# Kernel optimization log

Hardware: AMD Instinct MI355X
Metric: run time of the kernel (lower is better)

The kernel has to match this reference:

```python
import jax, jax.numpy as jnp
import numpy as np

N, B, E = 10000, 4, 160000
C_IN, C_OUT, C_E = 64, 64, 16


def _mk_params(key, c_in, c_out, c_e):
    ks = jax.random.split(key, 8)
    s = 0.1
    return dict(
        w_n=jax.random.normal(ks[0], (c_in, c_out), jnp.float32) * s,
        w_e=jax.random.normal(ks[1], (c_e, c_out), jnp.float32) * s,
        q=jax.random.normal(ks[2], (c_out, c_out), jnp.float32) * s,
        k=jax.random.normal(ks[3], (c_out, c_out), jnp.float32) * s,
        aw=jax.random.normal(ks[4], (3 * c_out, 1), jnp.float32) * s,
        ab=jax.random.normal(ks[5], (1,), jnp.float32) * s,
        ow=jax.random.normal(ks[6], (2 * c_out, c_out), jnp.float32) * s,
        ob=jax.random.normal(ks[7], (c_out,), jnp.float32) * s,
    )


def setup_inputs() -> dict:
    key = jax.random.key(0)
    kx, ke, ka, k1, k2 = jax.random.split(key, 5)
    inp = {
        'X': jax.random.normal(kx, (N, B, C_IN), jnp.float32),
        'edge_index': jax.random.randint(ke, (2, E), 0, N, jnp.int32),
        'edge_attr': jax.random.normal(ka, (E, C_E), jnp.float32),
    }
    p1 = _mk_params(k1, C_IN, C_OUT, C_E)
    p2 = _mk_params(k2, C_OUT, C_OUT, C_E)
    for name, v in p1.items():
        inp[name + '1'] = v
    for name, v in p2.items():
        inp[name + '2'] = v
    return inp


def egnn_conv(x, edge_index, edge_attr, w_n, w_e, q, k, aw, ab, ow, ob, n_nodes):
    # x: [N,B,Cin]; edge_attr: [E,Ce]
    xp = x @ w_n                         # [N,B,C]
    ea = edge_attr @ w_e                 # [E,C]
    src, dst = edge_index[0], edge_index[1]
    xj = xp[src]                         # [E,B,C] gather (source)
    xi = xp[dst]                         # [E,B,C] gather (target)
    qf = xj @ q                          # [E,B,C]
    kf = xi @ k                          # [E,B,C]
    eab = jnp.broadcast_to(ea[:, None, :], qf.shape)  # [E,B,C]
    att_feat = jnp.concatenate([qf, kf, eab], axis=-1)  # [E,B,3C]
    att = jax.nn.sigmoid(att_feat @ aw + ab)            # [E,B,1]
    gate = jax.nn.sigmoid(eab)
    msg = att * xj * gate                # [E,B,C]
    aggr = jax.ops.segment_max(msg, dst, num_segments=n_nodes)  # [N,B,C]
    aggr = jnp.where(jnp.isneginf(aggr), 0.0, aggr)  # empty segments -> 0
    out = jnp.concatenate([xp, aggr], axis=-1) @ ow + ob
    return xp + out


def reference(X, edge_index, edge_attr,
              w_n1, w_e1, q1, k1, aw1, ab1, ow1, ob1,
              w_n2, w_e2, q2, k2, aw2, ab2, ow2, ob2):
    n_nodes = X.shape[0]
    c1 = egnn_conv(X, edge_index, edge_attr, w_n1, w_e1, q1, k1, aw1, ab1, ow1, ob1, n_nodes)
    c1 = jax.nn.leaky_relu(c1, 0.01)
    c2 = egnn_conv(c1, edge_index, edge_attr, w_n2, w_e2, q2, k2, aw2, ab2, ow2, ob2, n_nodes)
    c2 = jax.nn.leaky_relu(c2, 0.01)
    return c2
```

## Files before the change

### kernel.cpp

```cpp
#include <hip/hip_runtime.h>
#include <math.h>

#define NN 10000
#define BB 4
#define EE 160000
#define CC 64
#define CE 16

static constexpr size_t OFF_XPA    = 0;
static constexpr size_t OFF_XPB    = 10240000;
static constexpr size_t OFF_SA     = 20480000;
static constexpr size_t OFF_SB     = 20640000;
static constexpr size_t OFF_VECS   = 20800000;
static constexpr size_t OFF_COUNTS = 20801280;
static constexpr size_t OFF_CURSOR = 20841280;
static constexpr size_t OFF_OFFS   = 20881280;
static constexpr size_t OFF_RECS   = 20921344;
static constexpr size_t OFF_ATT    = 22201344;
static constexpr size_t OFF_SE12   = 24761344;
static constexpr size_t OFF_ORDER  = 26041344;

__device__ __forceinline__ float sigmoidf_(float x) {
    return __builtin_amdgcn_rcpf(1.0f + __expf(-x));
}

__device__ __forceinline__ float bcast_(float v, int l) {
    return __uint_as_float(__builtin_amdgcn_readlane(__float_as_uint(v), l));
}

__global__ void hist_vecs_kernel(const int* __restrict__ ei, int* __restrict__ counts,
                                 const float* __restrict__ q1, const float* __restrict__ k1,
                                 const float* __restrict__ aw1, const float* __restrict__ we1,
                                 const float* __restrict__ q2, const float* __restrict__ k2,
                                 const float* __restrict__ aw2, const float* __restrict__ we2,
                                 float* __restrict__ vecs) {
    int e = blockIdx.x * blockDim.x + threadIdx.x;
    if (e < EE) atomicAdd(&counts[ei[EE + e]], 1);
    if (blockIdx.x == 0) {
        int t = threadIdx.x;
        if (t < 64) {
            float a = 0.f, b = 0.f, c = 0.f, d = 0.f;
            for (int j = 0; j < 64; ++j) {
                a = fmaf(q1[t * 64 + j], aw1[j], a);
                b = fmaf(k1[t * 64 + j], aw1[64 + j], b);
                c = fmaf(q2[t * 64 + j], aw2[j], c);
                d = fmaf(k2[t * 64 + j], aw2[64 + j], d);
            }
            vecs[t] = a; vecs[64 + t] = b; vecs[144 + t] = c; vecs[208 + t] = d;
        }
        if (t < 16) {
            float a = 0.f, b = 0.f;
            for (int j = 0; j < 64; ++j) {
                a = fmaf(we1[t * 64 + j], aw1[128 + j], a);
                b = fmaf(we2[t * 64 + j], aw2[128 + j], b);
            }
            vecs[128 + t] = a; vecs[272 + t] = b;
        }
    }
}

__global__ __launch_bounds__(1024) void scan_order_kernel(const int* __restrict__ counts,
                                                          int* __restrict__ offs,
                                                          int* __restrict__ order) {
    __shared__ int hist[1024];
    __shared__ int cur[1024];
    __shared__ int startb[1024];
    __shared__ int wsum[16];
    int t = threadIdx.x;
    hist[t] = 0; cur[t] = 0;
    int lane = t & 63, wid = t >> 6;
    int v[10];
    int s = 0;
    #pragma unroll
    for (int j = 0; j < 10; ++j) {
        int i = t * 10 + j;
        v[j] = (i < NN) ? counts[i] : 0;
        s += v[j];
    }
    int ps = s;
    #pragma unroll
    for (int off = 1; off < 64; off <<= 1) {
        int u = __shfl_up(ps, off, 64);
        if (lane >= off) ps += u;
    }
    if (lane == 63) wsum[wid] = ps;
    __syncthreads();
    int wbase = 0;
    for (int w = 0; w < wid; ++w) wbase += wsum[w];
    int tb = wbase + ps - s;
    #pragma unroll
    for (int j = 0; j < 10; ++j) {
        int i = t * 10 + j;
        if (i < NN) offs[i] = tb;
        tb += v[j];
    }
    if (t == 1023) offs[NN] = tb;
    #pragma unroll
    for (int j = 0; j < 10; ++j) {
        int i = t * 10 + j;
        if (i < NN) {
            int d = v[j] > 1023 ? 1023 : v[j];
            atomicAdd(&hist[d], 1);
        }
    }
    __syncthreads();
    int r = 1023 - t;
    int hv = hist[r];
    int ps2 = hv;
    #pragma unroll
    for (int off = 1; off < 64; off <<= 1) {
        int u = __shfl_up(ps2, off, 64);
        if (lane >= off) ps2 += u;
    }
    if (lane == 63) wsum[wid] = ps2;
    __syncthreads();
    int wb2 = 0;
    for (int w = 0; w < wid; ++w) wb2 += wsum[w];
    startb[r] = wb2 + ps2 - hv;
    __syncthreads();
    #pragma unroll
    for (int j = 0; j < 10; ++j) {
        int i = t * 10 + j;
        if (i < NN) {
            int d = v[j] > 1023 ? 1023 : v[j];
            int pos = startb[d] + atomicAdd(&cur[d], 1);
            order[pos] = i;
        }
    }
}

__global__ __launch_bounds__(256) void scatter_kernel(
    const int* __restrict__ ei, const int* __restrict__ offs,
    int* __restrict__ cursor, const float* __restrict__ attr,
    const float* __restrict__ vecs, const float* __restrict__ ab1,
    const float* __restrict__ ab2, int2* __restrict__ recs,
    float2* __restrict__ se12) {
    int e = blockIdx.x * blockDim.x + threadIdx.x;
    if (e >= EE) return;
    int s = ei[e], d = ei[EE + e];
    const float4* ap = (const float4*)(attr + (size_t)e * CE);
    float4 a0 = ap[0], a1 = ap[1], a2 = ap[2], a3 = ap[3];
    const float* v1 = vecs + 128;
    const float* v2 = vecs + 272;
    float s1 = ab1[0], s2 = ab2[0];
    s1 = fmaf(a0.x, v1[0], s1);  s1 = fmaf(a0.y, v1[1], s1);
    s1 = fmaf(a0.z, v1[2], s1);  s1 = fmaf(a0.w, v1[3], s1);
    s1 = fmaf(a1.x, v1[4], s1);  s1 = fmaf(a1.y, v1[5], s1);
    s1 = fmaf(a1.z, v1[6], s1);  s1 = fmaf(a1.w, v1[7], s1);
    s1 = fmaf(a2.x, v1[8], s1);  s1 = fmaf(a2.y, v1[9], s1);
    s1 = fmaf(a2.z, v1[10], s1); s1 = fmaf(a2.w, v1[11], s1);
    s1 = fmaf(a3.x, v1[12], s1); s1 = fmaf(a3.y, v1[13], s1);
    s1 = fmaf(a3.z, v1[14], s1); s1 = fmaf(a3.w, v1[15], s1);
    s2 = fmaf(a0.x, v2[0], s2);  s2 = fmaf(a0.y, v2[1], s2);
    s2 = fmaf(a0.z, v2[2], s2);  s2 = fmaf(a0.w, v2[3], s2);
    s2 = fmaf(a1.x, v2[4], s2);  s2 = fmaf(a1.y, v2[5], s2);
    s2 = fmaf(a1.z, v2[6], s2);  s2 = fmaf(a1.w, v2[7], s2);
    s2 = fmaf(a2.x, v2[8], s2);  s2 = fmaf(a2.y, v2[9], s2);
    s2 = fmaf(a2.z, v2[10], s2); s2 = fmaf(a2.w, v2[11], s2);
    s2 = fmaf(a3.x, v2[12], s2); s2 = fmaf(a3.y, v2[13], s2);
    s2 = fmaf(a3.z, v2[14], s2); s2 = fmaf(a3.w, v2[15], s2);
    int p = atomicAdd(&cursor[d], 1);
    recs[offs[d] + p] = make_int2(s, e);
    se12[e] = make_float2(s1, s2);
}

__global__ __launch_bounds__(256) void node_prep_kernel(
    const float* __restrict__ x, const float* __restrict__ w_n,
    const float* __restrict__ qa, const float* __restrict__ ka,
    float* __restrict__ xp, float* __restrict__ sa, float* __restrict__ sb) {
    __shared__ float w_sh[64 * 64];
    __shared__ float x_sh[4 * BB * CC];
    int t = threadIdx.x;
    for (int i = t; i < 64 * 64; i += 256) w_sh[i] = w_n[i];
    int node0 = blockIdx.x * 4;
    const float4* xg = (const float4*)(x + (size_t)node0 * BB * CC);
    ((float4*)x_sh)[t] = xg[t];
    __syncthreads();
    int wave = t >> 6, lane = t & 63;
    int node = node0 + wave;
    const float* xrow = x_sh + wave * BB * CC;
    float acc0 = 0.f, acc1 = 0.f, acc2 = 0.f, acc3 = 0.f;
    #pragma unroll 8
    for (int ci = 0; ci < 64; ++ci) {
        float w = w_sh[ci * 64 + lane];
        acc0 = fmaf(xrow[ci], w, acc0);
        acc1 = fmaf(xrow[64 + ci], w, acc1);
        acc2 = fmaf(xrow[128 + ci], w, acc2);
        acc3 = fmaf(xrow[192 + ci], w, acc3);
    }
    size_t obase = (size_t)node * BB * CC + lane;
    xp[obase] = acc0;
    xp[obase + 64] = acc1;
    xp[obase + 128] = acc2;
    xp[obase + 192] = acc3;
    float qv = qa[lane], kv = ka[lane];
    float ra0 = acc0 * qv, ra1 = acc1 * qv, ra2 = acc2 * qv, ra3 = acc3 * qv;
    float rb0 = acc0 * kv, rb1 = acc1 * kv, rb2 = acc2 * kv, rb3 = acc3 * kv;
    #pragma unroll
    for (int off = 32; off >= 1; off >>= 1) {
        ra0 += __shfl_xor(ra0, off, 64); ra1 += __shfl_xor(ra1, off, 64);
        ra2 += __shfl_xor(ra2, off, 64); ra3 += __shfl_xor(ra3, off, 64);
        rb0 += __shfl_xor(rb0, off, 64); rb1 += __shfl_xor(rb1, off, 64);
        rb2 += __shfl_xor(rb2, off, 64); rb3 += __shfl_xor(rb3, off, 64);
    }
    if (lane == 0) {
        sa[node * BB + 0] = ra0; sa[node * BB + 1] = ra1;
        sa[node * BB + 2] = ra2; sa[node * BB + 3] = ra3;
        sb[node * BB + 0] = rb0; sb[node * BB + 1] = rb1;
        sb[node * BB + 2] = rb2; sb[node * BB + 3] = rb3;
    }
}

__global__ __launch_bounds__(256) void att_kernel(
    const int* __restrict__ ei, const float2* __restrict__ se12,
    const float* __restrict__ sa, const float* __restrict__ sb,
    float4* __restrict__ att, int sel) {
    int e = blockIdx.x * blockDim.x + threadIdx.x;
    if (e >= EE) return;
    int s = ei[e], d = ei[EE + e];
    float2 se2 = se12[e];
    float se = sel ? se2.y : se2.x;
    float4 sas = *(const float4*)(sa + (size_t)s * BB);
    float4 sbn = *(const float4*)(sb + (size_t)d * BB);
    float4 r;
    r.x = sigmoidf_(sas.x + sbn.x + se);
    r.y = sigmoidf_(sas.y + sbn.y + se);
    r.z = sigmoidf_(sas.z + sbn.z + se);
    r.w = sigmoidf_(sas.w + sbn.w + se);
    att[e] = r;
}

__global__ __launch_bounds__(256) void conv_out_kernel(
    const float* __restrict__ xp,
    const int2* __restrict__ recs,
    const int* __restrict__ offs,
    const float* __restrict__ attr,
    const float* __restrict__ w_e,
    const float4* __restrict__ att,
    const float* __restrict__ ow,
    const float* __restrict__ ob,
    const int* __restrict__ order,
    float* __restrict__ out) {
    int t = threadIdx.x;
    int wave = t >> 6, lane = t & 63;
    int node = order[blockIdx.x * 4 + wave];

    float wec[CE];
    #pragma unroll
    for (int j = 0; j < CE; ++j) wec[j] = w_e[j * CC + lane];

    const float* xn = xp + (size_t)node * BB * CC + lane;
    float xn0 = xn[0], xn1 = xn[64], xn2 = xn[128], xn3 = xn[192];

    int o0 = offs[node], o1 = offs[node + 1];
    float m0 = -INFINITY, m1 = -INFINITY, m2 = -INFINITY, m3 = -INFINITY;

    int i = o0;
    int2 rec = (i < o1) ? recs[i] : make_int2(0, 0);
    while (i < o1) {
        int2 cur = rec;
        ++i;
        if (i < o1) rec = recs[i];
        int s = cur.x, e = cur.y;
        float4 at = att[e];
        const float4* ap = (const float4*)(attr + (size_t)e * CE);
        float4 a0 = ap[0], a1 = ap[1], a2 = ap[2], a3 = ap[3];
        float g = 0.f;
        g = fmaf(a0.x, wec[0], g);  g = fmaf(a0.y, wec[1], g);
        g = fmaf(a0.z, wec[2], g);  g = fmaf(a0.w, wec[3], g);
        g = fmaf(a1.x, wec[4], g);  g = fmaf(a1.y, wec[5], g);
        g = fmaf(a1.z, wec[6], g);  g = fmaf(a1.w, wec[7], g);
        g = fmaf(a2.x, wec[8], g);  g = fmaf(a2.y, wec[9], g);
        g = fmaf(a2.z, wec[10], g); g = fmaf(a2.w, wec[11], g);
        g = fmaf(a3.x, wec[12], g); g = fmaf(a3.y, wec[13], g);
        g = fmaf(a3.z, wec[14], g); g = fmaf(a3.w, wec[15], g);
        g = sigmoidf_(g);
        const float* xs = xp + (size_t)s * BB * CC + lane;
        float x0 = xs[0], x1 = xs[64], x2 = xs[128], x3 = xs[192];
        m0 = fmaxf(m0, at.x * x0 * g);
        m1 = fmaxf(m1, at.y * x1 * g);
        m2 = fmaxf(m2, at.z * x2 * g);
        m3 = fmaxf(m3, at.w * x3 * g);
    }
    m0 = (m0 == -INFINITY) ? 0.f : m0;
    m1 = (m1 == -INFINITY) ? 0.f : m1;
    m2 = (m2 == -INFINITY) ? 0.f : m2;
    m3 = (m3 == -INFINITY) ? 0.f : m3;

    float o0f = 0.f, o1f = 0.f, o2f = 0.f, o3f = 0.f;
    #pragma unroll
    for (int ci = 0; ci < 64; ++ci) {
        float wa = ow[ci * 64 + lane];
        float wb = ow[(64 + ci) * 64 + lane];
        o0f = fmaf(bcast_(xn0, ci), wa, o0f);
        o1f = fmaf(bcast_(xn1, ci), wa, o1f);
        o2f = fmaf(bcast_(xn2, ci), wa, o2f);
        o3f = fmaf(bcast_(xn3, ci), wa, o3f);
        o0f = fmaf(bcast_(m0, ci), wb, o0f);
        o1f = fmaf(bcast_(m1, ci), wb, o1f);
        o2f = fmaf(bcast_(m2, ci), wb, o2f);
        o3f = fmaf(bcast_(m3, ci), wb, o3f);
    }
    float obv = ob[lane];
    float r0 = xn0 + o0f + obv;
    float r1 = xn1 + o1f + obv;
    float r2 = xn2 + o2f + obv;
    float r3 = xn3 + o3f + obv;
    r0 = (r0 > 0.f) ? r0 : 0.01f * r0;
    r1 = (r1 > 0.f) ? r1 : 0.01f * r1;
    r2 = (r2 > 0.f) ? r2 : 0.01f * r2;
    r3 = (r3 > 0.f) ? r3 : 0.01f * r3;
    float* op = out + (size_t)node * BB * CC + lane;
    op[0] = r0; op[64] = r1; op[128] = r2; op[192] = r3;
}

extern "C" void kernel_launch(void* const* d_in, const int* in_sizes, int n_in,
                              void* d_out, int out_size, void* d_ws, size_t ws_size,
                              hipStream_t stream) {
    const float* X    = (const float*)d_in[0];
    const int*   ei   = (const int*)d_in[1];
    const float* attr = (const float*)d_in[2];
    const float* w_n1 = (const float*)d_in[3];
    const float* w_e1 = (const float*)d_in[4];
    const float* q1   = (const float*)d_in[5];
    const float* k1   = (const float*)d_in[6];
    const float* aw1  = (const float*)d_in[7];
    const float* ab1  = (const float*)d_in[8];
    const float* ow1  = (const float*)d_in[9];
    const float* ob1  = (const float*)d_in[10];
    const float* w_n2 = (const float*)d_in[11];
    const float* w_e2 = (const float*)d_in[12];
    const float* q2   = (const float*)d_in[13];
    const float* k2   = (const float*)d_in[14];
    const float* aw2  = (const float*)d_in[15];
    const float* ab2  = (const float*)d_in[16];
    const float* ow2  = (const float*)d_in[17];
    const float* ob2  = (const float*)d_in[18];
    float* out = (float*)d_out;

    char* ws = (char*)d_ws;
    float*  xpA    = (float*)(ws + OFF_XPA);
    float*  xpB    = (float*)(ws + OFF_XPB);
    float*  sa     = (float*)(ws + OFF_SA);
    float*  sb     = (float*)(ws + OFF_SB);
    float*  vecs   = (float*)(ws + OFF_VECS);
    int*    counts = (int*)(ws + OFF_COUNTS);
    int*    cursor = (int*)(ws + OFF_CURSOR);
    int*    offs   = (int*)(ws + OFF_OFFS);
    int2*   recs   = (int2*)(ws + OFF_RECS);
    float4* att    = (float4*)(ws + OFF_ATT);
    float2* se12   = (float2*)(ws + OFF_SE12);
    int*    order  = (int*)(ws + OFF_ORDER);

    hipMemsetAsync(counts, 0, 2 * NN * sizeof(int), stream);
    hist_vecs_kernel<<<EE / 256, 256, 0, stream>>>(ei, counts, q1, k1, aw1, w_e1,
                                                   q2, k2, aw2, w_e2, vecs);
    scan_order_kernel<<<1, 1024, 0, stream>>>(counts, offs, order);
    scatter_kernel<<<EE / 256, 256, 0, stream>>>(ei, offs, cursor, attr, vecs,
                                                 ab1, ab2, recs, se12);
    node_prep_kernel<<<NN / 4, 256, 0, stream>>>(X, w_n1, vecs + 0, vecs + 64, xpA, sa, sb);
    att_kernel<<<EE / 256, 256, 0, stream>>>(ei, se12, sa, sb, att, 0);
    conv_out_kernel<<<NN / 4, 256, 0, stream>>>(xpA, recs, offs, attr, w_e1, att,
                                                ow1, ob1, order, xpB);
    node_prep_kernel<<<NN / 4, 256, 0, stream>>>(xpB, w_n2, vecs + 144, vecs + 208, xpA, sa, sb);
    att_kernel<<<EE / 256, 256, 0, stream>>>(ei, se12, sa, sb, att, 1);
    conv_out_kernel<<<NN / 4, 256, 0, stream>>>(xpA, recs, offs, attr, w_e2, att,
                                                ow2, ob2, order, out);
}
```

Baseline: 285.1 us.

## Software-pipeline edge loads in conv_out and drop LDS staging in node_prep

The per-node edge loop in conv_out now uses two register buffers (A/B). The attention, edge-attribute and source-feature loads for the next two edges are issued before the current edge's gate and max are computed, which hides gather latency behind arithmetic. In node_prep, the LDS staging of w_n and x is removed: each lane loads a float4 of x into registers, the values are broadcast across lanes with bcast_, and weights are read straight from global/L1. This removes the __syncthreads and LDS traffic, but raises register pressure and adds a lane-broadcast per FMA group.

```diff
diff --git a/kernel.cpp b/kernel.cpp
--- a/kernel.cpp
+++ b/kernel.cpp
@@ -168,25 +168,20 @@
     const float* __restrict__ x, const float* __restrict__ w_n,
     const float* __restrict__ qa, const float* __restrict__ ka,
     float* __restrict__ xp, float* __restrict__ sa, float* __restrict__ sb) {
-    __shared__ float w_sh[64 * 64];
-    __shared__ float x_sh[4 * BB * CC];
-    int t = threadIdx.x;
-    for (int i = t; i < 64 * 64; i += 256) w_sh[i] = w_n[i];
-    int node0 = blockIdx.x * 4;
-    const float4* xg = (const float4*)(x + (size_t)node0 * BB * CC);
-    ((float4*)x_sh)[t] = xg[t];
-    __syncthreads();
-    int wave = t >> 6, lane = t & 63;
-    int node = node0 + wave;
-    const float* xrow = x_sh + wave * BB * CC;
+    int t = threadIdx.x, wave = t >> 6, lane = t & 63;
+    int node = blockIdx.x * 4 + wave;
+    float4 xv = ((const float4*)(x + (size_t)node * BB * CC))[lane];
     float acc0 = 0.f, acc1 = 0.f, acc2 = 0.f, acc3 = 0.f;
-    #pragma unroll 8
+    #pragma unroll
     for (int ci = 0; ci < 64; ++ci) {
-        float w = w_sh[ci * 64 + lane];
-        acc0 = fmaf(xrow[ci], w, acc0);
-        acc1 = fmaf(xrow[64 + ci], w, acc1);
-        acc2 = fmaf(xrow[128 + ci], w, acc2);
-        acc3 = fmaf(xrow[192 + ci], w, acc3);
+        float w = w_n[ci * 64 + lane];
+        float c0 = ((ci & 3) == 0) ? xv.x : ((ci & 3) == 1) ? xv.y
+                 : ((ci & 3) == 2) ? xv.z : xv.w;
+        int src = ci >> 2;
+        acc0 = fmaf(bcast_(c0, (0 << 4) | src), w, acc0);
+        acc1 = fmaf(bcast_(c0, (1 << 4) | src), w, acc1);
+        acc2 = fmaf(bcast_(c0, (2 << 4) | src), w, acc2);
+        acc3 = fmaf(bcast_(c0, (3 << 4) | src), w, acc3);
     }
     size_t obase = (size_t)node * BB * CC + lane;
     xp[obase] = acc0;
@@ -230,6 +225,29 @@
     att[e] = r;
 }
 
+#define CLOAD(R_, P) {                                                        \
+    P##at = att[(R_).y];                                                      \
+    const float4* ap_ = (const float4*)(attr + (size_t)(R_).y * CE);          \
+    P##a0 = ap_[0]; P##a1 = ap_[1]; P##a2 = ap_[2]; P##a3 = ap_[3];           \
+    const float* xs_ = xp + (size_t)(R_).x * (BB * CC) + lane;                \
+    P##x0 = xs_[0]; P##x1 = xs_[64]; P##x2 = xs_[128]; P##x3 = xs_[192]; }
+
+#define CCOMP(P) {                                                            \
+    float g_ = 0.f;                                                           \
+    g_ = fmaf(P##a0.x, wec[0], g_);  g_ = fmaf(P##a0.y, wec[1], g_);          \
+    g_ = fmaf(P##a0.z, wec[2], g_);  g_ = fmaf(P##a0.w, wec[3], g_);          \
+    g_ = fmaf(P##a1.x, wec[4], g_);  g_ = fmaf(P##a1.y, wec[5], g_);          \
+    g_ = fmaf(P##a1.z, wec[6], g_);  g_ = fmaf(P##a1.w, wec[7], g_);          \
+    g_ = fmaf(P##a2.x, wec[8], g_);  g_ = fmaf(P##a2.y, wec[9], g_);          \
+    g_ = fmaf(P##a2.z, wec[10], g_); g_ = fmaf(P##a2.w, wec[11], g_);         \
+    g_ = fmaf(P##a3.x, wec[12], g_); g_ = fmaf(P##a3.y, wec[13], g_);         \
+    g_ = fmaf(P##a3.z, wec[14], g_); g_ = fmaf(P##a3.w, wec[15], g_);         \
+    g_ = sigmoidf_(g_);                                                       \
+    m0 = fmaxf(m0, P##at.x * P##x0 * g_);                                     \
+    m1 = fmaxf(m1, P##at.y * P##x1 * g_);                                     \
+    m2 = fmaxf(m2, P##at.z * P##x2 * g_);                                     \
+    m3 = fmaxf(m3, P##at.w * P##x3 * g_); }
+
 __global__ __launch_bounds__(256) void conv_out_kernel(
     const float* __restrict__ xp,
     const int2* __restrict__ recs,
@@ -253,35 +271,27 @@
     float xn0 = xn[0], xn1 = xn[64], xn2 = xn[128], xn3 = xn[192];
 
     int o0 = offs[node], o1 = offs[node + 1];
+    int n = o1 - o0;
+    const int2* rp = recs + o0;
     float m0 = -INFINITY, m1 = -INFINITY, m2 = -INFINITY, m3 = -INFINITY;
 
-    int i = o0;
-    int2 rec = (i < o1) ? recs[i] : make_int2(0, 0);
-    while (i < o1) {
-        int2 cur = rec;
-        ++i;
-        if (i < o1) rec = recs[i];
-        int s = cur.x, e = cur.y;
-        float4 at = att[e];
-        const float4* ap = (const float4*)(attr + (size_t)e * CE);
-        float4 a0 = ap[0], a1 = ap[1], a2 = ap[2], a3 = ap[3];
-        float g = 0.f;
-        g = fmaf(a0.x, wec[0], g);  g = fmaf(a0.y, wec[1], g);
-        g = fmaf(a0.z, wec[2], g);  g = fmaf(a0.w, wec[3], g);
-        g = fmaf(a1.x, wec[4], g);  g = fmaf(a1.y, wec[5], g);
-        g = fmaf(a1.z, wec[6], g);  g = fmaf(a1.w, wec[7], g);
-        g = fmaf(a2.x, wec[8], g);  g = fmaf(a2.y, wec[9], g);
-        g = fmaf(a2.z, wec[10], g); g = fmaf(a2.w, wec[11], g);
-        g = fmaf(a3.x, wec[12], g); g = fmaf(a3.y, wec[13], g);
-        g = fmaf(a3.z, wec[14], g); g = fmaf(a3.w, wec[15], g);
-        g = sigmoidf_(g);
-        const float* xs = xp + (size_t)s * BB * CC + lane;
-        float x0 = xs[0], x1 = xs[64], x2 = xs[128], x3 = xs[192];
-        m0 = fmaxf(m0, at.x * x0 * g);
-        m1 = fmaxf(m1, at.y * x1 * g);
-        m2 = fmaxf(m2, at.z * x2 * g);
-        m3 = fmaxf(m3, at.w * x3 * g);
-    }
+    float4 Aat, Aa0, Aa1, Aa2, Aa3; float Ax0, Ax1, Ax2, Ax3;
+    float4 Bat, Ba0, Ba1, Ba2, Ba3; float Bx0, Bx1, Bx2, Bx3;
+    int2 rA = make_int2(0, 0), rB = rA;
+    if (n > 0) { rA = rp[0]; CLOAD(rA, A); }
+    if (n > 1) { rB = rp[1]; CLOAD(rB, B); }
+    int i = 0;
+    #pragma unroll 1
+    for (; i + 2 < n; i += 2) {
+        int2 rA2 = rp[i + 2];
+        int2 rB2 = (i + 3 < n) ? rp[i + 3] : rA2;
+        CCOMP(A);
+        rA = rA2; CLOAD(rA, A);
+        CCOMP(B);
+        rB = rB2; CLOAD(rB, B);
+    }
+    if (i < n)     CCOMP(A);
+    if (i + 1 < n) CCOMP(B);
     m0 = (m0 == -INFINITY) ? 0.f : m0;
     m1 = (m1 == -INFINITY) ? 0.f : m1;
     m2 = (m2 == -INFINITY) ? 0.f : m2;
```

After: 274.0 us. 3.9% less time.
